# Performance work log

Hardware: AMD Instinct MI355X
Metric: run time of the kernel (lower is better)

## Reference

```python
import jax, jax.numpy as jnp
import numpy as np


def _ln(z, g, b, eps=1e-5):
    mu = z.mean(-1, keepdims=True)
    v = ((z - mu) ** 2).mean(-1, keepdims=True)
    return (z - mu) / jnp.sqrt(v + eps) * g + b


def _forward(x, C_prev, n_prev, m_prev, ln_in_g, ln_in_b, wq, bq, wk, bk, wv, bv, wi, bi, wf, bf, wo, bo, rd_w1, rd_b1, rd_g, rd_be, rd_w2, rd_b2, ssm_log_lam, ssm_log_b, ssm_c, ssm_log_d, ssm_log_step, ssm_vol_gate, ssm_alpha, ssm_ln_g, ssm_ln_b, ln_mem_g, ln_mem_b):
    B, S, F = x.shape
    D = wq.shape[0]
    sqd = jnp.sqrt(jnp.float32(D))
    w = max(1, int(S * 0.2))
    pad0 = jnp.zeros((B, 1, F), x.dtype)
    cs = jnp.concatenate([pad0, jnp.cumsum(x, 1)], 1)
    cs2 = jnp.concatenate([pad0, jnp.cumsum(x * x, 1)], 1)
    wsum = cs[:, w:] - cs[:, :-w]
    wsq = cs2[:, w:] - cs2[:, :-w]
    var = (wsq - wsum * wsum / w) / (w - 1)
    std = jnp.sqrt(jnp.clip(var, 0.0))
    vol = jnp.concatenate([jnp.broadcast_to(std[:, :1], (B, w - 1, F)), std], 1)
    sv = vol.mean(2, keepdims=True)
    sv = sv / (sv.mean(1, keepdims=True) + 1e-6)  # [B,S,1]
    # --- parallel gate computation ---
    xn = _ln(x, ln_in_g, ln_in_b)
    regime = jax.nn.softmax(jax.nn.gelu(_ln(xn @ rd_w1.T + rd_b1, rd_g, rd_be), approximate=False) @ rd_w2.T + rd_b2, axis=-1)
    q = xn @ wq.T + bq
    k = (xn @ wk.T + bk) / sqd
    v = xn @ wv.T + bv
    it = xn @ wi.T + bi  # [B,S,1]
    ft = xn @ wf.T + bf
    o = jax.nn.sigmoid(xn @ wo.T + bo)
    # --- stabilize_gates (running-max exponential stabilization) ---
    mp = jnp.clip(m_prev, -100.0, 100.0)[:, None, :]  # [B,1,1]
    m_t = jnp.maximum(ft, mp + ft)
    ig = jnp.exp(jnp.clip(it - m_t, -15.0, 15.0))
    fg = jnp.exp(jnp.clip(ft + mp - m_t, -15.0, 15.0))
    # --- store_key_value outer products + cumulative matrix memory ---
    kn = k / (jnp.linalg.norm(k, axis=2, keepdims=True) + 1e-12) * sqd
    vn = v / (jnp.linalg.norm(v, axis=2, keepdims=True) + 1e-6) * sqd
    upd = jnp.clip(ig, 0.0, 1.0)[..., None] * (vn[..., :, None] * kn[..., None, :])  # [B,S,D,D]
    f_cum = jnp.cumprod(fg, axis=1)  # [B,S,1]
    C_t = f_cum[..., None] * C_prev[:, None] + jnp.cumsum(upd, 1)
    # --- structured state-space mixing, vectorized over the D memory rows ---
    lam = -jnp.exp(ssm_log_lam)
    step = jnp.exp(ssm_log_step)
    a_disc = (2.0 + step * lam) / (2.0 - step * lam)  # bilinear discretization
    b_disc = step * (1.0 + a_disc) * jnp.exp(ssm_log_b)[:, 0] / 2.0
    xr = C_t.transpose(0, 2, 1, 3).reshape(B * D, S, D)  # rows folded into batch
    volr = jnp.broadcast_to(sv[:, None, :, 0], (B, D, S)).reshape(B * D, S)
    u = xr.mean(-1)  # [BD,S], per-step scalar drive
    vgate = jax.nn.sigmoid(ssm_vol_gate)
    def stepf(h, inp):
        u_t, vol_t = inp
        h = a_disc[None] * h + b_disc[None] * u_t[:, None]
        h = _ln(h, ssm_ln_g, ssm_ln_b)
        h = h / (1.0 + vgate[None] * vol_t[:, None])
        return h, h
    h0 = jnp.zeros((B * D, D), x.dtype)
    _, hs = jax.lax.scan(stepf, h0, (u.T, volr.T))  # [S,BD,D]
    yscal = jnp.einsum('sbn,n->bs', hs, ssm_c[0])  # [BD,S]
    y = yscal[..., None] + jnp.exp(ssm_log_d) * xr
    alpha = jax.nn.sigmoid(ssm_alpha)
    mixed = alpha * xr + (1.0 - alpha) * y
    C_mixed = mixed.reshape(B, D, S, D).transpose(0, 2, 1, 3)
    mf = regime[:, :, 0:1][..., None]  # regime-aware mixing factor
    C_t = C_mixed * mf + C_t * (1.0 - mf)
    C_t = C_t / (jnp.linalg.norm(C_t.reshape(B, S, D * D), axis=-1)[..., None, None] + 1e-6) * sqd
    # --- mLSTM readout (stabilizer_threshold = 1.0) ---
    n_t = f_cum * n_prev[:, None, :] + jnp.cumsum(ig * k, 1)
    h_til = jnp.einsum('bsij,bsj->bsi', C_t, q)
    denom = jnp.maximum(jnp.abs(jnp.sum(n_t * q, -1, keepdims=True)), 1.0)
    return o * _ln(h_til / denom, ln_mem_g, ln_mem_b)


def setup_inputs() -> dict:
    key = jax.random.key(0)
    ks = jax.random.split(key, 12)
    B, S, F, D = 8, 512, 32, 64
    sF, sD = 1.0 / np.sqrt(F), 1.0 / np.sqrt(D)
    n = lambda k, sh, s=1.0: jax.random.normal(k, sh, jnp.float32) * s
    return dict(
        x=n(ks[0], (B, S, F)),
        C_prev=jnp.zeros((B, D, D), jnp.float32),
        n_prev=jnp.zeros((B, D), jnp.float32),
        m_prev=jnp.zeros((B, 1), jnp.float32),
        ln_in_g=jnp.ones((F,), jnp.float32), ln_in_b=jnp.zeros((F,), jnp.float32),
        wq=n(ks[1], (D, F), sF), bq=jnp.zeros((D,), jnp.float32),
        wk=n(ks[2], (D, F), sF), bk=jnp.zeros((D,), jnp.float32),
        wv=n(ks[3], (D, F), sF), bv=jnp.zeros((D,), jnp.float32),
        wi=n(ks[4], (1, F), sF), bi=jnp.zeros((1,), jnp.float32),
        wf=n(ks[5], (1, F), sF), bf=jnp.ones((1,), jnp.float32),
        wo=n(ks[6], (D, F), sF), bo=jnp.zeros((D,), jnp.float32),
        rd_w1=n(ks[7], (D, F), sF), rd_b1=jnp.zeros((D,), jnp.float32),
        rd_g=jnp.ones((D,), jnp.float32), rd_be=jnp.zeros((D,), jnp.float32),
        rd_w2=n(ks[8], (4, D), sD), rd_b2=jnp.zeros((4,), jnp.float32),
        ssm_log_lam=jnp.linspace(np.log(0.001), np.log(0.1), D).astype(jnp.float32),
        ssm_log_b=jax.random.uniform(ks[9], (D, 1), jnp.float32, -0.5, 0.5),
        ssm_c=n(ks[10], (1, D), sD),
        ssm_log_d=jnp.zeros((1,), jnp.float32),
        ssm_log_step=jnp.float32(np.log(0.001)),
        ssm_vol_gate=jnp.ones((D,), jnp.float32),
        ssm_alpha=jnp.float32(0.7),
        ssm_ln_g=jnp.ones((D,), jnp.float32), ssm_ln_b=jnp.zeros((D,), jnp.float32),
        ln_mem_g=jnp.ones((D,), jnp.float32), ln_mem_b=jnp.zeros((D,), jnp.float32),
    )


def reference(x, C_prev, n_prev, m_prev, ln_in_g, ln_in_b, wq, bq, wk, bk, wv, bv, wi, bi, wf, bf, wo, bo, rd_w1, rd_b1, rd_g, rd_be, rd_w2, rd_b2, ssm_log_lam, ssm_log_b, ssm_c, ssm_log_d, ssm_log_step, ssm_vol_gate, ssm_alpha, ssm_ln_g, ssm_ln_b, ln_mem_g, ln_mem_b):
    return _forward(x, C_prev, n_prev, m_prev, ln_in_g, ln_in_b, wq, bq, wk, bk, wv, bv, wi, bi, wf, bf, wo, bo, rd_w1, rd_b1, rd_g, rd_be, rd_w2, rd_b2, ssm_log_lam, ssm_log_b, ssm_c, ssm_log_d, ssm_log_step, ssm_vol_gate, ssm_alpha, ssm_ln_g, ssm_ln_b, ln_mem_g, ln_mem_b)
```

## Files before the change

kernel.cpp:

```cpp
#include <hip/hip_runtime.h>
#include <math.h>

#define BB 8
#define SS 512
#define FF 32
#define DD 64
#define WVOL 102
#define CH 16
#define NCH (SS / CH)
#define QR 4

template<int CTRL, int RM, bool BC>
__device__ __forceinline__ float updpp(float oldv, float x) {
  return __int_as_float(__builtin_amdgcn_update_dpp(
      __float_as_int(oldv), __float_as_int(x), CTRL, RM, 0xF, BC));
}
__device__ __forceinline__ float rlane(float v, int l) {
  return __int_as_float(__builtin_amdgcn_readlane(__float_as_int(v), l));
}
__device__ __forceinline__ float dsum64(float x) {
  x += updpp<0x111, 0xF, true>(0.f, x);
  x += updpp<0x112, 0xF, true>(0.f, x);
  x += updpp<0x114, 0xF, true>(0.f, x);
  x += updpp<0x118, 0xF, true>(0.f, x);
  x += updpp<0x142, 0xF, true>(0.f, x);
  x += updpp<0x143, 0xF, true>(0.f, x);
  return rlane(x, 63);
}
__device__ __forceinline__ float dsum32(float x) {
  x += updpp<0x111, 0xF, true>(0.f, x);
  x += updpp<0x112, 0xF, true>(0.f, x);
  x += updpp<0x114, 0xF, true>(0.f, x);
  x += updpp<0x118, 0xF, true>(0.f, x);
  x += updpp<0x142, 0xF, true>(0.f, x);
  return rlane(x, 31);
}
__device__ __forceinline__ float dscan_add(float x) {
  x += updpp<0x111, 0xF, true>(0.f, x);
  x += updpp<0x112, 0xF, true>(0.f, x);
  x += updpp<0x114, 0xF, true>(0.f, x);
  x += updpp<0x118, 0xF, true>(0.f, x);
  x += updpp<0x142, 0xA, true>(0.f, x);
  x += updpp<0x143, 0xC, true>(0.f, x);
  return x;
}
__device__ __forceinline__ float dscan_mul(float x) {
  x *= updpp<0x111, 0xF, false>(1.f, x);
  x *= updpp<0x112, 0xF, false>(1.f, x);
  x *= updpp<0x114, 0xF, false>(1.f, x);
  x *= updpp<0x118, 0xF, false>(1.f, x);
  x *= updpp<0x142, 0xA, false>(1.f, x);
  x *= updpp<0x143, 0xC, false>(1.f, x);
  return x;
}

__global__ void k_prep(const float* __restrict__ Cp,
                       const float* __restrict__ wq, const float* __restrict__ wk,
                       const float* __restrict__ wv, const float* __restrict__ wo,
                       const float* __restrict__ rw1,
                       float* __restrict__ CpT, float* __restrict__ wqT,
                       float* __restrict__ wkT, float* __restrict__ wvT,
                       float* __restrict__ woT, float* __restrict__ rw1T,
                       float* __restrict__ cpr, float* __restrict__ cpn2) {
  int blk = blockIdx.x; int lane = threadIdx.x;
  if (blk < BB) {
    int b = blk;
    const float* rowp = Cp + (size_t)(b * DD + lane) * DD;
    float rs = 0.f, r2 = 0.f;
#pragma unroll 8
    for (int j = 0; j < DD; ++j) {
      float c = rowp[j];
      rs += c; r2 = fmaf(c, c, r2);
      CpT[(size_t)(b * DD + j) * DD + lane] = c;
    }
    cpr[b * DD + lane] = rs;
    float tot2 = dsum64(r2);
    if (lane == 0) cpn2[b] = tot2;
  } else {
    const float* src; float* dst;
    switch (blk - BB) {
      case 0: src = wq;  dst = wqT;  break;
      case 1: src = wk;  dst = wkT;  break;
      case 2: src = wv;  dst = wvT;  break;
      case 3: src = wo;  dst = woT;  break;
      default: src = rw1; dst = rw1T; break;
    }
#pragma unroll 8
    for (int f = 0; f < FF; ++f) dst[f * DD + lane] = src[lane * FF + f];
  }
}

__global__ void k_vol_std(const float* __restrict__ x, float* __restrict__ svraw) {
  int b = blockIdx.x; int s = WVOL - 1 + blockIdx.y;
  int lane = threadIdx.x; int f = lane & 31; int half = lane >> 5;
  const float* xb = x + (size_t)(b * SS) * FF + f;
  float wsum = 0.f, wsq = 0.f;
  int t0 = s - WVOL + 1 + half;
#pragma unroll 17
  for (int k = 0; k < WVOL / 2; ++k) {
    float xv = xb[(t0 + 2 * k) * FF];
    wsum += xv; wsq = fmaf(xv, xv, wsq);
  }
  wsum += __shfl_xor(wsum, 32); wsq += __shfl_xor(wsq, 32);
  float var = (wsq - wsum * wsum * (1.f / WVOL)) * (1.f / (WVOL - 1));
  float sd = sqrtf(fmaxf(var, 0.f));
  float m = dsum64(sd) * 0.5f * (1.f / FF);
  if (lane == 0) svraw[b * SS + s] = m;
}

__global__ void k_proj(const float* __restrict__ x, const float* __restrict__ m_prev,
                       const float* __restrict__ CpT,
                       const float* __restrict__ ln_in_g, const float* __restrict__ ln_in_b,
                       const float* __restrict__ wqT, const float* __restrict__ bq,
                       const float* __restrict__ wkT, const float* __restrict__ bk,
                       const float* __restrict__ wvT, const float* __restrict__ bv,
                       const float* __restrict__ wi, const float* __restrict__ bi,
                       const float* __restrict__ wf, const float* __restrict__ bf,
                       const float* __restrict__ woT, const float* __restrict__ bo,
                       const float* __restrict__ rw1T, const float* __restrict__ rd_b1,
                       const float* __restrict__ rd_g, const float* __restrict__ rd_be,
                       const float* __restrict__ rd_w2, const float* __restrict__ rd_b2,
                       float* __restrict__ qo, float* __restrict__ kno, float* __restrict__ vno,
                       float* __restrict__ iko, float* __restrict__ oo,
                       float* __restrict__ knT, float* __restrict__ vnT,
                       float* __restrict__ cg_a, float* __restrict__ fg_a,
                       float* __restrict__ mf_a, float* __restrict__ cks_a,
                       float* __restrict__ qsum_a, float* __restrict__ zc) {
  int bs = blockIdx.x; int b = bs / SS; int s = bs % SS;
  int lane = threadIdx.x;
  __shared__ float xs[FF];
  __shared__ float ks[DD];
  float xv = (lane < FF) ? x[bs * FF + lane] : 0.f;
  float s1x = dsum32(xv);
  float s2x = dsum32(xv * xv);
  if (lane < FF) {
    float mu = s1x * (1.f / FF);
    float var = s2x * (1.f / FF) - mu * mu;
    xs[lane] = (xv - mu) * rsqrtf(var + 1e-5f) * ln_in_g[lane] + ln_in_b[lane];
  }
  __syncthreads();
  int d = lane;
  float aq = bq[d], ak = bk[d], av = bv[d], ao = bo[d], at = rd_b1[d];
#pragma unroll
  for (int f = 0; f < FF; ++f) {
    float xf = xs[f];
    aq = fmaf(xf, wqT[f * DD + d], aq);
    ak = fmaf(xf, wkT[f * DD + d], ak);
    av = fmaf(xf, wvT[f * DD + d], av);
    ao = fmaf(xf, woT[f * DD + d], ao);
    at = fmaf(xf, rw1T[f * DD + d], at);
  }
  float pit = (lane < FF) ? xs[lane] * wi[lane] : 0.f;
  float pft = (lane < FF) ? xs[lane] * wf[lane] : 0.f;
  float itv = dsum32(pit) + bi[0];
  float ftv = dsum32(pft) + bf[0];
  float s1 = dsum64(at), s2 = dsum64(at * at);
  float mu = s1 * (1.f / DD);
  float var = s2 * (1.f / DD) - mu * mu;
  float tn = (at - mu) * rsqrtf(var + 1e-5f) * rd_g[d] + rd_be[d];
  float ge = 0.5f * tn * (1.f + erff(tn * 0.70710678118654752f));
  float l0 = dsum64(ge * rd_w2[0 * DD + d]) + rd_b2[0];
  float l1 = dsum64(ge * rd_w2[1 * DD + d]) + rd_b2[1];
  float l2 = dsum64(ge * rd_w2[2 * DD + d]) + rd_b2[2];
  float l3 = dsum64(ge * rd_w2[3 * DD + d]) + rd_b2[3];
  float mx = fmaxf(fmaxf(l0, l1), fmaxf(l2, l3));
  float e0 = expf(l0 - mx), e1 = expf(l1 - mx), e2 = expf(l2 - mx), e3 = expf(l3 - mx);
  float mfv = e0 / (e0 + e1 + e2 + e3);
  float kd = ak * 0.125f;
  float kk = dsum64(kd * kd);
  float knd = kd * (8.f / (sqrtf(kk) + 1e-12f));
  float vv = dsum64(av * av);
  float vnd = av * (8.f / (sqrtf(vv) + 1e-6f));
  float ksum = dsum64(knd);
  float qsum = dsum64(aq);
  float mp = fminf(fmaxf(m_prev[b], -100.f), 100.f);
  float mt = fmaxf(ftv, mp + ftv);
  float ig = expf(fminf(fmaxf(itv - mt, -15.f), 15.f));
  float fg = expf(fminf(fmaxf(ftv + mp - mt, -15.f), 15.f));
  float cg = fminf(ig, 1.f);
  qo[bs * DD + d] = aq;
  kno[bs * DD + d] = knd;
  vno[bs * DD + d] = vnd;
  iko[bs * DD + d] = ig * kd;
  oo[bs * DD + d] = 1.f / (1.f + expf(-ao));
  knT[(b * DD + d) * SS + s] = knd;
  vnT[(b * DD + d) * SS + s] = vnd;
  ks[d] = knd;
  __syncthreads();
  float acc = 0.f;
  const float* cpt = CpT + (size_t)b * DD * DD;
#pragma unroll 8
  for (int j = 0; j < DD; ++j) acc = fmaf(cpt[j * DD + d], ks[j], acc);
  float z = dsum64(vnd * acc);
  if (lane == 0) {
    cg_a[bs] = cg; fg_a[bs] = fg; mf_a[bs] = mfv;
    cks_a[bs] = cg * ksum; qsum_a[bs] = qsum;
    zc[bs] = cg * z;
  }
}

__global__ void k_main(const float* __restrict__ qo, const float* __restrict__ kno,
                       const float* __restrict__ vno,
                       const float* __restrict__ knT, const float* __restrict__ vnT,
                       const float* __restrict__ cg_a,
                       float* __restrict__ p2, float* __restrict__ rho) {
  int blk = blockIdx.x;
  int b = blk >> 7;
  int q0 = blk & 127;
  int qt = (q0 & 1) ? (127 - (q0 >> 1)) : (q0 >> 1);
  int lane = threadIdx.x;
  int s0 = qt * QR;
  __shared__ float vls[64][DD];
  __shared__ float qs[QR][DD], kss[QR][DD], vss[QR][DD];
  __shared__ float wl[64];
#pragma unroll
  for (int r = 0; r < QR; ++r) {
    int base = (b * SS + s0 + r) * DD + lane;
    qs[r][lane] = qo[base]; kss[r][lane] = kno[base]; vss[r][lane] = vno[base];
  }
  float p2a[QR], rhoa[QR], A[QR], G1[QR], G2[QR];
#pragma unroll
  for (int r = 0; r < QR; ++r) { p2a[r] = 0.f; rhoa[r] = 0.f; }
  int tmax = s0 + QR - 1;
  for (int t0 = 0; t0 <= tmax; t0 += 64) {
    int t = t0 + lane;
#pragma unroll 8
    for (int r = 0; r < 64; ++r) vls[r][lane] = vno[(b * SS + t0 + r) * DD + lane];
#pragma unroll
    for (int r = 0; r < QR; ++r) { A[r] = 0.f; G1[r] = 0.f; G2[r] = 0.f; }
    const float* kTp = knT + (size_t)b * DD * SS + t;
    const float* vTp = vnT + (size_t)b * DD * SS + t;
    for (int j = 0; j < DD; j += 4) {
      float kv0 = kTp[(j + 0) * SS], kv1 = kTp[(j + 1) * SS];
      float kv2 = kTp[(j + 2) * SS], kv3 = kTp[(j + 3) * SS];
      float vv0 = vTp[(j + 0) * SS], vv1 = vTp[(j + 1) * SS];
      float vv2 = vTp[(j + 2) * SS], vv3 = vTp[(j + 3) * SS];
#pragma unroll
      for (int r = 0; r < QR; ++r) {
        float4 qq = *(const float4*)&qs[r][j];
        float4 kk = *(const float4*)&kss[r][j];
        float4 vv = *(const float4*)&vss[r][j];
        A[r] = fmaf(kv0, qq.x, A[r]); A[r] = fmaf(kv1, qq.y, A[r]);
        A[r] = fmaf(kv2, qq.z, A[r]); A[r] = fmaf(kv3, qq.w, A[r]);
        G1[r] = fmaf(kv0, kk.x, G1[r]); G1[r] = fmaf(kv1, kk.y, G1[r]);
        G1[r] = fmaf(kv2, kk.z, G1[r]); G1[r] = fmaf(kv3, kk.w, G1[r]);
        G2[r] = fmaf(vv0, vv.x, G2[r]); G2[r] = fmaf(vv1, vv.y, G2[r]);
        G2[r] = fmaf(vv2, vv.z, G2[r]); G2[r] = fmaf(vv3, vv.w, G2[r]);
      }
    }
    float cgt = cg_a[b * SS + t];
#pragma unroll
    for (int r = 0; r < QR; ++r) {
      int s = s0 + r;
      float wr = (t < s) ? 2.f : (t == s ? 1.f : 0.f);
      rhoa[r] = fmaf(wr * cgt, G1[r] * G2[r], rhoa[r]);
    }
#pragma unroll
    for (int r = 0; r < QR; ++r) {
      int s = s0 + r;
      wl[lane] = (t <= s) ? cgt * A[r] : 0.f;
      float acc = p2a[r];
#pragma unroll 4
      for (int tt = 0; tt < 64; tt += 4) {
        float4 w4 = *(const float4*)&wl[tt];
        acc = fmaf(w4.x, vls[tt + 0][lane], acc);
        acc = fmaf(w4.y, vls[tt + 1][lane], acc);
        acc = fmaf(w4.z, vls[tt + 2][lane], acc);
        acc = fmaf(w4.w, vls[tt + 3][lane], acc);
      }
      p2a[r] = acc;
    }
  }
#pragma unroll
  for (int r = 0; r < QR; ++r) p2[(b * SS + s0 + r) * DD + lane] = p2a[r];
#pragma unroll
  for (int r = 0; r < QR; ++r) {
    float rr = dsum64(rhoa[r]);
    float cgs = cg_a[b * SS + s0 + r];
    if (lane == 0) rho[b * SS + s0 + r] = cgs * rr;
  }
}

__global__ void k_post(const float* __restrict__ fg_a, const float* __restrict__ zc,
                       const float* __restrict__ rho, const float* __restrict__ svraw,
                       const float* __restrict__ ik, const float* __restrict__ vno,
                       const float* __restrict__ cks_a,
                       float* __restrict__ fcum, float* __restrict__ cpd,
                       float* __restrict__ sn2, float* __restrict__ sv,
                       float* __restrict__ csn, float* __restrict__ csr) {
  int blk = blockIdx.x; int lane = threadIdx.x;
  if (blk < BB) {
    int b = blk;
    float m0 = svraw[b * SS + WVOL - 1];
    float vals[8]; float part = 0.f;
#pragma unroll
    for (int c = 0; c < 8; ++c) {
      int idx = c * 64 + lane;
      float v = (idx < WVOL - 1) ? m0 : svraw[b * SS + idx];
      vals[c] = v; part += v;
    }
    float tot = dsum64(part);
    float inv = 1.f / (tot * (1.f / SS) + 1e-6f);
#pragma unroll
    for (int c = 0; c < 8; ++c) sv[b * SS + c * 64 + lane] = vals[c] * inv;
    float cf = 1.f, cz = 0.f, crr = 0.f;
    for (int c = 0; c < 8; ++c) {
      int bs = b * SS + c * 64 + lane;
      float f = dscan_mul(fg_a[bs]) * cf;
      float z = dscan_add(zc[bs]) + cz;
      float r = dscan_add(rho[bs]) + crr;
      fcum[bs] = f; cpd[bs] = z; sn2[bs] = r;
      cf = rlane(f, 63); cz = rlane(z, 63); crr = rlane(r, 63);
    }
  } else {
    int blk2 = blk - BB; int b = blk2 / NCH; int w = blk2 % NCH; int d = lane;
    float na = 0.f, ra = 0.f;
#pragma unroll
    for (int t = 0; t < CH; ++t) {
      int bs = b * SS + w * CH + t;
      na += ik[bs * DD + d];
      ra = fmaf(cks_a[bs], vno[bs * DD + d], ra);
    }
    csn[blk2 * DD + d] = na; csr[blk2 * DD + d] = ra;
  }
}

__global__ void k_scan_apply(const float* __restrict__ ik, const float* __restrict__ vno,
                             const float* __restrict__ cks_a,
                             const float* __restrict__ csn, const float* __restrict__ csr,
                             float* __restrict__ nacc, float* __restrict__ racc) {
  int blk = blockIdx.x; int b = blk / NCH; int w = blk % NCH; int d = threadIdx.x;
  float na = 0.f, ra = 0.f;
  for (int w2 = 0; w2 < w; ++w2) {
    na += csn[(b * NCH + w2) * DD + d];
    ra += csr[(b * NCH + w2) * DD + d];
  }
#pragma unroll
  for (int t = 0; t < CH; ++t) {
    int bs = b * SS + w * CH + t;
    na += ik[bs * DD + d];
    ra = fmaf(cks_a[bs], vno[bs * DD + d], ra);
    nacc[bs * DD + d] = na;
    racc[bs * DD + d] = ra;
  }
}

__global__ void k_ssm(const float* __restrict__ fcum, const float* __restrict__ racc,
                      const float* __restrict__ cpr, const float* __restrict__ sv,
                      const float* __restrict__ log_lam, const float* __restrict__ log_b,
                      const float* __restrict__ cvec,
                      const float* __restrict__ log_step, const float* __restrict__ vol_gate,
                      const float* __restrict__ ln_g, const float* __restrict__ ln_b,
                      float* __restrict__ ysT) {
  int blk = blockIdx.x; int b = blk >> 6; int i = blk & 63;
  int n = threadIdx.x;
  float st = expf(log_step[0]);
  float lam = -expf(log_lam[n]);
  float ad = (2.f + st * lam) / (2.f - st * lam);
  float bd = st * (1.f + ad) * expf(log_b[n]) * 0.5f;
  float vg = 1.f / (1.f + expf(-vol_gate[n]));
  float g = ln_g[n], be = ln_b[n], cn = cvec[n];
  float cprv = cpr[b * DD + i];
  float u[8], w[8];
#pragma unroll
  for (int c = 0; c < 8; ++c) {
    int s = c * 64 + n; int bs = b * SS + s;
    u[c] = fmaf(fcum[bs], cprv, racc[(size_t)bs * DD + i]) * (1.f / DD);
    w[c] = sv[bs];
  }
  float h = 0.f;
#pragma unroll
  for (int c = 0; c < 8; ++c) {
    float yout = 0.f;
#pragma unroll 4
    for (int t = 0; t < 64; ++t) {
      float uu = rlane(u[c], t);
      float vv = rlane(w[c], t);
      float bdu = bd * uu;
      float rden = __builtin_amdgcn_rcpf(fmaf(vg, vv, 1.f));
      float grden = g * rden, berden = be * rden;
      float ht = fmaf(ad, h, bdu);
      float p1 = ht, p2 = ht * ht;
      p1 += updpp<0x111, 0xF, true>(0.f, p1); p2 += updpp<0x111, 0xF, true>(0.f, p2);
      p1 += updpp<0x112, 0xF, true>(0.f, p1); p2 += updpp<0x112, 0xF, true>(0.f, p2);
      p1 += updpp<0x114, 0xF, true>(0.f, p1); p2 += updpp<0x114, 0xF, true>(0.f, p2);
      p1 += updpp<0x118, 0xF, true>(0.f, p1); p2 += updpp<0x118, 0xF, true>(0.f, p2);
      p1 += updpp<0x142, 0xF, true>(0.f, p1); p2 += updpp<0x142, 0xF, true>(0.f, p2);
      p1 += updpp<0x143, 0xF, true>(0.f, p1); p2 += updpp<0x143, 0xF, true>(0.f, p2);
      float s1 = rlane(p1, 63), s2 = rlane(p2, 63);
      float mu = s1 * (1.f / DD);
      float r2m = fmaf(-mu, s1, s2);
      float arg = fmaxf(fmaf(r2m, 1.f / DD, 1e-5f), 1e-5f);
      float irs = __builtin_amdgcn_rsqf(arg);
      float hv = fmaf((ht - mu) * grden, irs, berden);
      h = hv;
      float y = cn * hv;
      y += updpp<0x111, 0xF, true>(0.f, y);
      y += updpp<0x112, 0xF, true>(0.f, y);
      y += updpp<0x114, 0xF, true>(0.f, y);
      y += updpp<0x118, 0xF, true>(0.f, y);
      y += updpp<0x142, 0xF, true>(0.f, y);
      y += updpp<0x143, 0xF, true>(0.f, y);
      float su = rlane(y, 63);
      yout = (n == t) ? su : yout;
    }
    ysT[(size_t)(b * DD + i) * SS + c * 64 + n] = yout;
  }
}

__global__ void k_final(const float* __restrict__ qo, const float* __restrict__ oo,
                        const float* __restrict__ p2, const float* __restrict__ racc,
                        const float* __restrict__ nacc, const float* __restrict__ ysT,
                        const float* __restrict__ CpT, const float* __restrict__ cpr,
                        const float* __restrict__ cpn2,
                        const float* __restrict__ fcum, const float* __restrict__ cpd,
                        const float* __restrict__ sn2,
                        const float* __restrict__ mf_a, const float* __restrict__ qsum_a,
                        const float* __restrict__ n_prev,
                        const float* __restrict__ ssm_log_d, const float* __restrict__ ssm_alpha,
                        const float* __restrict__ ln_mem_g, const float* __restrict__ ln_mem_b,
                        float* __restrict__ out) {
  int bs = blockIdx.x; int b = bs / SS; int s = bs % SS;
  int i = threadIdx.x;
  __shared__ float qv[DD];
  float qi = qo[bs * DD + i];
  qv[i] = qi;
  __syncthreads();
  float P1 = 0.f;
  const float* cpt = CpT + (size_t)b * DD * DD;
#pragma unroll 8
  for (int j = 0; j < DD; ++j) P1 = fmaf(cpt[j * DD + i], qv[j], P1);
  float fc = fcum[bs];
  float p = fmaf(fc, P1, p2[bs * DD + i]);
  float r = fmaf(fc, cpr[b * DD + i], racc[bs * DD + i]);
  float R2 = fc * fc * cpn2[b] + 2.f * fc * cpd[bs] + sn2[bs];
  float al = 1.f / (1.f + expf(-ssm_alpha[0]));
  float kap = al + (1.f - al) * expf(ssm_log_d[0]);
  float mfv = mf_a[bs];
  float beta = 1.f + mfv * (kap - 1.f);
  float gam = mfv * (1.f - al);
  float y = ysT[(size_t)(b * DD + i) * SS + s];
  float syr = dsum64(y * r);
  float sy2 = dsum64(y * y);
  float nrm2 = fmaxf(beta * beta * R2 + 2.f * beta * gam * syr + gam * gam * (float)DD * sy2, 0.f);
  float scale = 8.f / (sqrtf(nrm2) + 1e-6f);
  float nt = fmaf(fc, n_prev[b * DD + i], nacc[bs * DD + i]);
  float ndp = dsum64(nt * qi);
  float denom = fmaxf(fabsf(ndp), 1.f);
  float hh = scale * (fmaf(beta, p, gam * y * qsum_a[bs])) / denom;
  float s1 = dsum64(hh), s2 = dsum64(hh * hh);
  float mu = s1 * (1.f / DD);
  float var = fmaxf(s2 * (1.f / DD) - mu * mu, 0.f);
  float o = (hh - mu) * rsqrtf(var + 1e-5f) * ln_mem_g[i] + ln_mem_b[i];
  out[bs * DD + i] = oo[bs * DD + i] * o;
}

extern "C" void kernel_launch(void* const* d_in, const int* in_sizes, int n_in,
                              void* d_out, int out_size, void* d_ws, size_t ws_size,
                              hipStream_t stream) {
  const float* x        = (const float*)d_in[0];
  const float* C_prev   = (const float*)d_in[1];
  const float* n_prev   = (const float*)d_in[2];
  const float* m_prev   = (const float*)d_in[3];
  const float* ln_in_g  = (const float*)d_in[4];
  const float* ln_in_b  = (const float*)d_in[5];
  const float* wq = (const float*)d_in[6];  const float* bq = (const float*)d_in[7];
  const float* wk = (const float*)d_in[8];  const float* bk = (const float*)d_in[9];
  const float* wv = (const float*)d_in[10]; const float* bv = (const float*)d_in[11];
  const float* wi = (const float*)d_in[12]; const float* bi = (const float*)d_in[13];
  const float* wf = (const float*)d_in[14]; const float* bf = (const float*)d_in[15];
  const float* wo = (const float*)d_in[16]; const float* bo = (const float*)d_in[17];
  const float* rd_w1 = (const float*)d_in[18]; const float* rd_b1 = (const float*)d_in[19];
  const float* rd_g  = (const float*)d_in[20]; const float* rd_be = (const float*)d_in[21];
  const float* rd_w2 = (const float*)d_in[22]; const float* rd_b2 = (const float*)d_in[23];
  const float* ssm_log_lam  = (const float*)d_in[24];
  const float* ssm_log_b    = (const float*)d_in[25];
  const float* ssm_c        = (const float*)d_in[26];
  const float* ssm_log_d    = (const float*)d_in[27];
  const float* ssm_log_step = (const float*)d_in[28];
  const float* ssm_vol_gate = (const float*)d_in[29];
  const float* ssm_alpha    = (const float*)d_in[30];
  const float* ssm_ln_g     = (const float*)d_in[31];
  const float* ssm_ln_b     = (const float*)d_in[32];
  const float* ln_mem_g     = (const float*)d_in[33];
  const float* ln_mem_b     = (const float*)d_in[34];
  float* out = (float*)d_out;

  float* W = (float*)d_ws;
  size_t o0 = 0;
  const size_t BS = (size_t)BB * SS, BSD = BS * DD;
  float* sv    = W + o0; o0 += BS;
  float* svraw = W + o0; o0 += BS;
  float* qo   = W + o0; o0 += BSD;
  float* kno  = W + o0; o0 += BSD;
  float* vno  = W + o0; o0 += BSD;
  float* iko  = W + o0; o0 += BSD;
  float* oo   = W + o0; o0 += BSD;
  float* knT  = W + o0; o0 += BSD;
  float* vnT  = W + o0; o0 += BSD;
  float* p2   = W + o0; o0 += BSD;
  float* racc = W + o0; o0 += BSD;
  float* nacc = W + o0; o0 += BSD;
  float* ysT  = W + o0; o0 += BSD;
  float* cg_a = W + o0; o0 += BS;
  float* fg_a = W + o0; o0 += BS;
  float* mf_a = W + o0; o0 += BS;
  float* cks  = W + o0; o0 += BS;
  float* qsum = W + o0; o0 += BS;
  float* zc   = W + o0; o0 += BS;
  float* fcum = W + o0; o0 += BS;
  float* cpd  = W + o0; o0 += BS;
  float* rho  = W + o0; o0 += BS;
  float* sn2  = W + o0; o0 += BS;
  float* cpr  = W + o0; o0 += (size_t)BB * DD;
  float* cpn2 = W + o0; o0 += BB;
  float* csn  = W + o0; o0 += (size_t)BB * NCH * DD;
  float* csr  = W + o0; o0 += (size_t)BB * NCH * DD;
  float* CpT  = W + o0; o0 += (size_t)BB * DD * DD;
  float* wqT  = W + o0; o0 += (size_t)FF * DD;
  float* wkT  = W + o0; o0 += (size_t)FF * DD;
  float* wvT  = W + o0; o0 += (size_t)FF * DD;
  float* woT  = W + o0; o0 += (size_t)FF * DD;
  float* rw1T = W + o0; o0 += (size_t)FF * DD;

  hipLaunchKernelGGL(k_prep, dim3(BB + 5), dim3(64), 0, stream,
                     C_prev, wq, wk, wv, wo, rd_w1,
                     CpT, wqT, wkT, wvT, woT, rw1T, cpr, cpn2);
  hipLaunchKernelGGL(k_vol_std, dim3(BB, SS - WVOL + 1), dim3(64), 0, stream, x, svraw);
  hipLaunchKernelGGL(k_proj, dim3(BB * SS), dim3(64), 0, stream,
                     x, m_prev, CpT, ln_in_g, ln_in_b, wqT, bq, wkT, bk, wvT, bv, wi, bi,
                     wf, bf, woT, bo, rw1T, rd_b1, rd_g, rd_be, rd_w2, rd_b2,
                     qo, kno, vno, iko, oo, knT, vnT, cg_a, fg_a, mf_a, cks, qsum, zc);
  hipLaunchKernelGGL(k_main, dim3(BB * 128), dim3(64), 0, stream,
                     qo, kno, vno, knT, vnT, cg_a, p2, rho);
  hipLaunchKernelGGL(k_post, dim3(BB + BB * NCH), dim3(64), 0, stream,
                     fg_a, zc, rho, svraw, iko, vno, cks,
                     fcum, cpd, sn2, sv, csn, csr);
  hipLaunchKernelGGL(k_scan_apply, dim3(BB * NCH), dim3(64), 0, stream,
                     iko, vno, cks, csn, csr, nacc, racc);
  hipLaunchKernelGGL(k_ssm, dim3(BB * DD), dim3(64), 0, stream,
                     fcum, racc, cpr, sv, ssm_log_lam, ssm_log_b, ssm_c,
                     ssm_log_step, ssm_vol_gate, ssm_ln_g, ssm_ln_b, ysT);
  hipLaunchKernelGGL(k_final, dim3(BB * SS), dim3(64), 0, stream,
                     qo, oo, p2, racc, nacc, ysT, CpT, cpr, cpn2, fcum, cpd, sn2,
                     mf_a, qsum, n_prev, ssm_log_d, ssm_alpha, ln_mem_g, ln_mem_b, out);
}
```

Before: 342.4 us.

## Split causal attention into tiled QK and PV kernels with register blocking

Replaces the single k_main kernel, one 64-thread block per four query rows, with two kernels. k_qk computes 32x32 triangular tiles of the q·k, k·k and v·v Gram products using 256-thread blocks with 2x2 register blocking. It writes a masked, gated weight matrix W to global memory and accumulates rho with atomics. k_pv multiplies W by V in 64-column chunks, balancing the triangular work across blocks and accumulating p2 atomically; the transposed knT/vnT writes are dropped and the W/p2/rho buffers must be memset first. This raises data reuse and occupancy but adds a large B×S×S intermediate, a memset, and atomic traffic.

```diff
diff --git a/kernel.cpp b/kernel.cpp
--- a/kernel.cpp
+++ b/kernel.cpp
@@ -8,7 +8,6 @@
 #define WVOL 102
 #define CH 16
 #define NCH (SS / CH)
-#define QR 4
 
 template<int CTRL, int RM, bool BC>
 __device__ __forceinline__ float updpp(float oldv, float x) {
@@ -34,6 +33,13 @@
   x += updpp<0x118, 0xF, true>(0.f, x);
   x += updpp<0x142, 0xF, true>(0.f, x);
   return rlane(x, 31);
+}
+__device__ __forceinline__ float dsum16(float x) {
+  x += updpp<0x111, 0xF, true>(0.f, x);
+  x += updpp<0x112, 0xF, true>(0.f, x);
+  x += updpp<0x114, 0xF, true>(0.f, x);
+  x += updpp<0x118, 0xF, true>(0.f, x);
+  return x;
 }
 __device__ __forceinline__ float dscan_add(float x) {
   x += updpp<0x111, 0xF, true>(0.f, x);
@@ -122,11 +128,10 @@
                        const float* __restrict__ rd_w2, const float* __restrict__ rd_b2,
                        float* __restrict__ qo, float* __restrict__ kno, float* __restrict__ vno,
                        float* __restrict__ iko, float* __restrict__ oo,
-                       float* __restrict__ knT, float* __restrict__ vnT,
                        float* __restrict__ cg_a, float* __restrict__ fg_a,
                        float* __restrict__ mf_a, float* __restrict__ cks_a,
                        float* __restrict__ qsum_a, float* __restrict__ zc) {
-  int bs = blockIdx.x; int b = bs / SS; int s = bs % SS;
+  int bs = blockIdx.x; int b = bs / SS;
   int lane = threadIdx.x;
   __shared__ float xs[FF];
   __shared__ float ks[DD];
@@ -183,8 +188,6 @@
   vno[bs * DD + d] = vnd;
   iko[bs * DD + d] = ig * kd;
   oo[bs * DD + d] = 1.f / (1.f + expf(-ao));
-  knT[(b * DD + d) * SS + s] = knd;
-  vnT[(b * DD + d) * SS + s] = vnd;
   ks[d] = knd;
   __syncthreads();
   float acc = 0.f;
@@ -199,86 +202,139 @@
   }
 }
 
-__global__ void k_main(const float* __restrict__ qo, const float* __restrict__ kno,
-                       const float* __restrict__ vno,
-                       const float* __restrict__ knT, const float* __restrict__ vnT,
-                       const float* __restrict__ cg_a,
-                       float* __restrict__ p2, float* __restrict__ rho) {
-  int blk = blockIdx.x;
-  int b = blk >> 7;
-  int q0 = blk & 127;
-  int qt = (q0 & 1) ? (127 - (q0 >> 1)) : (q0 >> 1);
-  int lane = threadIdx.x;
-  int s0 = qt * QR;
-  __shared__ float vls[64][DD];
-  __shared__ float qs[QR][DD], kss[QR][DD], vss[QR][DD];
-  __shared__ float wl[64];
-#pragma unroll
-  for (int r = 0; r < QR; ++r) {
-    int base = (b * SS + s0 + r) * DD + lane;
-    qs[r][lane] = qo[base]; kss[r][lane] = kno[base]; vss[r][lane] = vno[base];
-  }
-  float p2a[QR], rhoa[QR], A[QR], G1[QR], G2[QR];
-#pragma unroll
-  for (int r = 0; r < QR; ++r) { p2a[r] = 0.f; rhoa[r] = 0.f; }
-  int tmax = s0 + QR - 1;
-  for (int t0 = 0; t0 <= tmax; t0 += 64) {
-    int t = t0 + lane;
-#pragma unroll 8
-    for (int r = 0; r < 64; ++r) vls[r][lane] = vno[(b * SS + t0 + r) * DD + lane];
-#pragma unroll
-    for (int r = 0; r < QR; ++r) { A[r] = 0.f; G1[r] = 0.f; G2[r] = 0.f; }
-    const float* kTp = knT + (size_t)b * DD * SS + t;
-    const float* vTp = vnT + (size_t)b * DD * SS + t;
-    for (int j = 0; j < DD; j += 4) {
-      float kv0 = kTp[(j + 0) * SS], kv1 = kTp[(j + 1) * SS];
-      float kv2 = kTp[(j + 2) * SS], kv3 = kTp[(j + 3) * SS];
-      float vv0 = vTp[(j + 0) * SS], vv1 = vTp[(j + 1) * SS];
-      float vv2 = vTp[(j + 2) * SS], vv3 = vTp[(j + 3) * SS];
-#pragma unroll
-      for (int r = 0; r < QR; ++r) {
-        float4 qq = *(const float4*)&qs[r][j];
-        float4 kk = *(const float4*)&kss[r][j];
-        float4 vv = *(const float4*)&vss[r][j];
-        A[r] = fmaf(kv0, qq.x, A[r]); A[r] = fmaf(kv1, qq.y, A[r]);
-        A[r] = fmaf(kv2, qq.z, A[r]); A[r] = fmaf(kv3, qq.w, A[r]);
-        G1[r] = fmaf(kv0, kk.x, G1[r]); G1[r] = fmaf(kv1, kk.y, G1[r]);
-        G1[r] = fmaf(kv2, kk.z, G1[r]); G1[r] = fmaf(kv3, kk.w, G1[r]);
-        G2[r] = fmaf(vv0, vv.x, G2[r]); G2[r] = fmaf(vv1, vv.y, G2[r]);
-        G2[r] = fmaf(vv2, vv.z, G2[r]); G2[r] = fmaf(vv3, vv.w, G2[r]);
+__global__ void k_qk(const float* __restrict__ qo, const float* __restrict__ kno,
+                     const float* __restrict__ vno, const float* __restrict__ cg_a,
+                     float* __restrict__ W, float* __restrict__ rho) {
+  int blk = blockIdx.x; int b = blk / 136; int r = blk % 136;
+  int st = 0;
+  while ((st + 1) * (st + 2) / 2 <= r) ++st;
+  int tt = r - st * (st + 1) / 2;
+  int s0 = st * 32, t0 = tt * 32;
+  int tid = threadIdx.x; int ty = tid >> 4, tx = tid & 15;
+  __shared__ float qls[32][64], kls[32][64], vsl[32][64];
+  __shared__ float ktl[32][68], vtl[32][68];
+  __shared__ float cgl[32], sacc[32];
+  {
+    int col = tid & 63, rg = tid >> 6;
+#pragma unroll
+    for (int rr = 0; rr < 8; ++rr) {
+      int row = rg * 8 + rr;
+      int gi = (b * SS + s0 + row) * DD + col;
+      int gj = (b * SS + t0 + row) * DD + col;
+      qls[row][col] = qo[gi]; kls[row][col] = kno[gi]; vsl[row][col] = vno[gi];
+      ktl[row][col] = kno[gj]; vtl[row][col] = vno[gj];
+    }
+    if (tid < 32) cgl[tid] = cg_a[b * SS + t0 + tid];
+  }
+  __syncthreads();
+  float A[2][2] = {{0.f, 0.f}, {0.f, 0.f}};
+  float KK[2][2] = {{0.f, 0.f}, {0.f, 0.f}};
+  float VV[2][2] = {{0.f, 0.f}, {0.f, 0.f}};
+  for (int k4 = 0; k4 < DD; k4 += 4) {
+    float qa[2][4], ka[2][4], va[2][4], kt[2][4], vt[2][4];
+#pragma unroll
+    for (int i = 0; i < 2; ++i) {
+      float4 t1 = *(const float4*)&qls[ty * 2 + i][k4];
+      qa[i][0] = t1.x; qa[i][1] = t1.y; qa[i][2] = t1.z; qa[i][3] = t1.w;
+      float4 t2 = *(const float4*)&kls[ty * 2 + i][k4];
+      ka[i][0] = t2.x; ka[i][1] = t2.y; ka[i][2] = t2.z; ka[i][3] = t2.w;
+      float4 t3 = *(const float4*)&vsl[ty * 2 + i][k4];
+      va[i][0] = t3.x; va[i][1] = t3.y; va[i][2] = t3.z; va[i][3] = t3.w;
+      float4 t4 = *(const float4*)&ktl[tx * 2 + i][k4];
+      kt[i][0] = t4.x; kt[i][1] = t4.y; kt[i][2] = t4.z; kt[i][3] = t4.w;
+      float4 t5 = *(const float4*)&vtl[tx * 2 + i][k4];
+      vt[i][0] = t5.x; vt[i][1] = t5.y; vt[i][2] = t5.z; vt[i][3] = t5.w;
+    }
+#pragma unroll
+    for (int kk = 0; kk < 4; ++kk)
+#pragma unroll
+      for (int i = 0; i < 2; ++i)
+#pragma unroll
+        for (int j = 0; j < 2; ++j) {
+          A[i][j]  = fmaf(qa[i][kk], kt[j][kk], A[i][j]);
+          KK[i][j] = fmaf(ka[i][kk], kt[j][kk], KK[i][j]);
+          VV[i][j] = fmaf(va[i][kk], vt[j][kk], VV[i][j]);
+        }
+  }
+  float cg0 = cgl[tx * 2], cg1 = cgl[tx * 2 + 1];
+  int tg0 = t0 + tx * 2, tg1 = t0 + tx * 2 + 1;
+#pragma unroll
+  for (int i = 0; i < 2; ++i) {
+    int s = s0 + ty * 2 + i;
+    float w0 = (tg0 <= s) ? cg0 * A[i][0] : 0.f;
+    float w1 = (tg1 <= s) ? cg1 * A[i][1] : 0.f;
+    float2 wst = make_float2(w0, w1);
+    *(float2*)&W[((size_t)b * SS + s) * SS + tg0] = wst;
+    float wr0 = (tg0 < s) ? 2.f : (tg0 == s ? 1.f : 0.f);
+    float wr1 = (tg1 < s) ? 2.f : (tg1 == s ? 1.f : 0.f);
+    float rsum = dsum16(fmaf(wr0 * cg0, KK[i][0] * VV[i][0],
+                             wr1 * cg1 * KK[i][1] * VV[i][1]));
+    if (tx == 15) sacc[ty * 2 + i] = rsum;
+  }
+  __syncthreads();
+  if (tid < 32) {
+    int s = s0 + tid;
+    atomicAdd(&rho[b * SS + s], cg_a[b * SS + s] * sacc[tid]);
+  }
+}
+
+__global__ void k_pv(const float* __restrict__ W, const float* __restrict__ vno,
+                     float* __restrict__ p2) {
+  int blk = blockIdx.x; int b = blk / 26; int u = blk % 26;
+  int st32, c0, c1;
+  if (u < 6) { st32 = u; c0 = 0; c1 = u >> 1; }
+  else {
+    int v = u - 6; st32 = 6 + (v >> 1);
+    int nch = (st32 >> 1) + 1; int h0 = nch >> 1;
+    if (v & 1) { c0 = h0; c1 = nch - 1; } else { c0 = 0; c1 = h0 - 1; }
+  }
+  int s0 = st32 * 32;
+  int tid = threadIdx.x; int ty = tid >> 4, tx = tid & 15;
+  __shared__ float wls[32][64];
+  __shared__ float vls[64][64];
+  float acc[2][4] = {{0.f, 0.f, 0.f, 0.f}, {0.f, 0.f, 0.f, 0.f}};
+  for (int c = c0; c <= c1; ++c) {
+    __syncthreads();
+    int t0 = c * 64;
+    int col = tid & 63, rg = tid >> 6;
+#pragma unroll
+    for (int rr = 0; rr < 8; ++rr) {
+      int r2 = rg * 8 + rr;
+      wls[r2][col] = W[((size_t)b * SS + s0 + r2) * SS + t0 + col];
+    }
+#pragma unroll
+    for (int rr = 0; rr < 16; ++rr) {
+      int t = rg * 16 + rr;
+      vls[t][col] = vno[(b * SS + t0 + t) * DD + col];
+    }
+    __syncthreads();
+    for (int k4 = 0; k4 < 64; k4 += 4) {
+      float aa[2][4];
+#pragma unroll
+      for (int i = 0; i < 2; ++i) {
+        float4 t1 = *(const float4*)&wls[ty * 2 + i][k4];
+        aa[i][0] = t1.x; aa[i][1] = t1.y; aa[i][2] = t1.z; aa[i][3] = t1.w;
       }
-    }
-    float cgt = cg_a[b * SS + t];
-#pragma unroll
-    for (int r = 0; r < QR; ++r) {
-      int s = s0 + r;
-      float wr = (t < s) ? 2.f : (t == s ? 1.f : 0.f);
-      rhoa[r] = fmaf(wr * cgt, G1[r] * G2[r], rhoa[r]);
-    }
-#pragma unroll
-    for (int r = 0; r < QR; ++r) {
-      int s = s0 + r;
-      wl[lane] = (t <= s) ? cgt * A[r] : 0.f;
-      float acc = p2a[r];
-#pragma unroll 4
-      for (int tt = 0; tt < 64; tt += 4) {
-        float4 w4 = *(const float4*)&wl[tt];
-        acc = fmaf(w4.x, vls[tt + 0][lane], acc);
-        acc = fmaf(w4.y, vls[tt + 1][lane], acc);
-        acc = fmaf(w4.z, vls[tt + 2][lane], acc);
-        acc = fmaf(w4.w, vls[tt + 3][lane], acc);
+      float bb[4][4];
+#pragma unroll
+      for (int kk = 0; kk < 4; ++kk) {
+        float4 t2 = *(const float4*)&vls[k4 + kk][tx * 4];
+        bb[kk][0] = t2.x; bb[kk][1] = t2.y; bb[kk][2] = t2.z; bb[kk][3] = t2.w;
       }
-      p2a[r] = acc;
-    }
-  }
-#pragma unroll
-  for (int r = 0; r < QR; ++r) p2[(b * SS + s0 + r) * DD + lane] = p2a[r];
-#pragma unroll
-  for (int r = 0; r < QR; ++r) {
-    float rr = dsum64(rhoa[r]);
-    float cgs = cg_a[b * SS + s0 + r];
-    if (lane == 0) rho[b * SS + s0 + r] = cgs * rr;
-  }
+#pragma unroll
+      for (int kk = 0; kk < 4; ++kk)
+#pragma unroll
+        for (int i = 0; i < 2; ++i)
+#pragma unroll
+          for (int j = 0; j < 4; ++j)
+            acc[i][j] = fmaf(aa[i][kk], bb[kk][j], acc[i][j]);
+    }
+  }
+#pragma unroll
+  for (int i = 0; i < 2; ++i)
+#pragma unroll
+    for (int j = 0; j < 4; ++j)
+      atomicAdd(&p2[(b * SS + s0 + ty * 2 + i) * DD + tx * 4 + j], acc[i][j]);
 }
 
 __global__ void k_post(const float* __restrict__ fg_a, const float* __restrict__ zc,
@@ -486,43 +542,43 @@
   const float* ln_mem_b     = (const float*)d_in[34];
   float* out = (float*)d_out;
 
-  float* W = (float*)d_ws;
+  float* Wsp = (float*)d_ws;
   size_t o0 = 0;
-  const size_t BS = (size_t)BB * SS, BSD = BS * DD;
-  float* sv    = W + o0; o0 += BS;
-  float* svraw = W + o0; o0 += BS;
-  float* qo   = W + o0; o0 += BSD;
-  float* kno  = W + o0; o0 += BSD;
-  float* vno  = W + o0; o0 += BSD;
-  float* iko  = W + o0; o0 += BSD;
-  float* oo   = W + o0; o0 += BSD;
-  float* knT  = W + o0; o0 += BSD;
-  float* vnT  = W + o0; o0 += BSD;
-  float* p2   = W + o0; o0 += BSD;
-  float* racc = W + o0; o0 += BSD;
-  float* nacc = W + o0; o0 += BSD;
-  float* ysT  = W + o0; o0 += BSD;
-  float* cg_a = W + o0; o0 += BS;
-  float* fg_a = W + o0; o0 += BS;
-  float* mf_a = W + o0; o0 += BS;
-  float* cks  = W + o0; o0 += BS;
-  float* qsum = W + o0; o0 += BS;
-  float* zc   = W + o0; o0 += BS;
-  float* fcum = W + o0; o0 += BS;
-  float* cpd  = W + o0; o0 += BS;
-  float* rho  = W + o0; o0 += BS;
-  float* sn2  = W + o0; o0 += BS;
-  float* cpr  = W + o0; o0 += (size_t)BB * DD;
-  float* cpn2 = W + o0; o0 += BB;
-  float* csn  = W + o0; o0 += (size_t)BB * NCH * DD;
-  float* csr  = W + o0; o0 += (size_t)BB * NCH * DD;
-  float* CpT  = W + o0; o0 += (size_t)BB * DD * DD;
-  float* wqT  = W + o0; o0 += (size_t)FF * DD;
-  float* wkT  = W + o0; o0 += (size_t)FF * DD;
-  float* wvT  = W + o0; o0 += (size_t)FF * DD;
-  float* woT  = W + o0; o0 += (size_t)FF * DD;
-  float* rw1T = W + o0; o0 += (size_t)FF * DD;
-
+  const size_t BS = (size_t)BB * SS, BSD = BS * DD, WSZ = (size_t)BB * SS * SS;
+  float* sv    = Wsp + o0; o0 += BS;
+  float* svraw = Wsp + o0; o0 += BS;
+  float* qo   = Wsp + o0; o0 += BSD;
+  float* kno  = Wsp + o0; o0 += BSD;
+  float* vno  = Wsp + o0; o0 += BSD;
+  float* iko  = Wsp + o0; o0 += BSD;
+  float* oo   = Wsp + o0; o0 += BSD;
+  float* racc = Wsp + o0; o0 += BSD;
+  float* nacc = Wsp + o0; o0 += BSD;
+  float* ysT  = Wsp + o0; o0 += BSD;
+  float* p2   = Wsp + o0; o0 += BSD;
+  float* rho  = Wsp + o0; o0 += BS;
+  float* Wm   = Wsp + o0; o0 += WSZ;
+  float* cg_a = Wsp + o0; o0 += BS;
+  float* fg_a = Wsp + o0; o0 += BS;
+  float* mf_a = Wsp + o0; o0 += BS;
+  float* cks  = Wsp + o0; o0 += BS;
+  float* qsum = Wsp + o0; o0 += BS;
+  float* zc   = Wsp + o0; o0 += BS;
+  float* fcum = Wsp + o0; o0 += BS;
+  float* cpd  = Wsp + o0; o0 += BS;
+  float* sn2  = Wsp + o0; o0 += BS;
+  float* cpr  = Wsp + o0; o0 += (size_t)BB * DD;
+  float* cpn2 = Wsp + o0; o0 += BB;
+  float* csn  = Wsp + o0; o0 += (size_t)BB * NCH * DD;
+  float* csr  = Wsp + o0; o0 += (size_t)BB * NCH * DD;
+  float* CpT  = Wsp + o0; o0 += (size_t)BB * DD * DD;
+  float* wqT  = Wsp + o0; o0 += (size_t)FF * DD;
+  float* wkT  = Wsp + o0; o0 += (size_t)FF * DD;
+  float* wvT  = Wsp + o0; o0 += (size_t)FF * DD;
+  float* woT  = Wsp + o0; o0 += (size_t)FF * DD;
+  float* rw1T = Wsp + o0; o0 += (size_t)FF * DD;
+
+  hipMemsetAsync(p2, 0, (BSD + BS + WSZ) * sizeof(float), stream);
   hipLaunchKernelGGL(k_prep, dim3(BB + 5), dim3(64), 0, stream,
                      C_prev, wq, wk, wv, wo, rd_w1,
                      CpT, wqT, wkT, wvT, woT, rw1T, cpr, cpn2);
@@ -530,9 +586,10 @@
   hipLaunchKernelGGL(k_proj, dim3(BB * SS), dim3(64), 0, stream,
                      x, m_prev, CpT, ln_in_g, ln_in_b, wqT, bq, wkT, bk, wvT, bv, wi, bi,
                      wf, bf, woT, bo, rw1T, rd_b1, rd_g, rd_be, rd_w2, rd_b2,
-                     qo, kno, vno, iko, oo, knT, vnT, cg_a, fg_a, mf_a, cks, qsum, zc);
-  hipLaunchKernelGGL(k_main, dim3(BB * 128), dim3(64), 0, stream,
-                     qo, kno, vno, knT, vnT, cg_a, p2, rho);
+                     qo, kno, vno, iko, oo, cg_a, fg_a, mf_a, cks, qsum, zc);
+  hipLaunchKernelGGL(k_qk, dim3(BB * 136), dim3(256), 0, stream,
+                     qo, kno, vno, cg_a, Wm, rho);
+  hipLaunchKernelGGL(k_pv, dim3(BB * 26), dim3(256), 0, stream, Wm, vno, p2);
   hipLaunchKernelGGL(k_post, dim3(BB + BB * NCH), dim3(64), 0, stream,
                      fg_a, zc, rho, svraw, iko, vno, cks,
                      fcum, cpd, sn2, sv, csn, csr);
```

New measurement: 295.1 us. -13.8%, faster.
